# Performance work log

Measured on AMD Instinct MI355X. Metric: run time of the kernel, lower is better.

Reference implementation:

```python
import jax, jax.numpy as jnp
import numpy as np

N = 50000          # nodes
E = 800000         # edges (before self-loops)
IN = 128           # in_dim
HID = 128          # hidden_dim
HEADS = 4
G = 256            # graphs in batch
EPS = 1e-5         # batchnorm eps
NEG_SLOPE = 0.2    # GATConv leaky_relu slope


def _gat_layer(x, src, dst, W, a_src, a_dst, bias, H, C, concat):
    """PyG-style GATConv (self-loops already appended to src/dst)."""
    n = x.shape[0]
    h = (x @ W).reshape(n, H, C)                       # [N,H,C]
    s_src = (h * a_src).sum(-1)                        # [N,H]
    s_dst = (h * a_dst).sum(-1)                        # [N,H]
    e = jax.nn.leaky_relu(s_src[src] + s_dst[dst], NEG_SLOPE)   # [E',H]
    m = jax.ops.segment_max(e, dst, num_segments=n)    # segment-wise softmax
    ex = jnp.exp(e - m[dst])
    den = jax.ops.segment_sum(ex, dst, num_segments=n)
    alpha = ex / den[dst]                              # [E',H]
    out = jax.ops.segment_sum(alpha[..., None] * h[src], dst, num_segments=n)  # [N,H,C]
    out = out.reshape(n, H * C) if concat else out.mean(axis=1)
    return out + bias


def _bn(x, gamma, beta):
    # PyG BatchNorm over nodes (training-mode batch statistics)
    mu = x.mean(axis=0)
    var = x.var(axis=0)
    return gamma * (x - mu) * jax.lax.rsqrt(var + EPS) + beta


def setup_inputs() -> dict:
    key = jax.random.key(0)
    ks = jax.random.split(key, 32)
    d = {}
    d["x"] = jax.random.normal(ks[0], (N, IN), dtype=jnp.float32)
    d["edge_index"] = jax.random.randint(ks[1], (2, E), 0, N, dtype=jnp.int64)
    d["batch_idx"] = jnp.sort(jax.random.randint(ks[2], (N,), 0, G, dtype=jnp.int64))
    dims = [(IN, HEADS, HID, True), (HID * HEADS, HEADS, HID, True), (HID * HEADS, 1, HID, False)]
    for i, (din, H, C, concat) in enumerate(dims):
        d[f"W{i}"] = jax.random.normal(ks[3 + 4 * i], (din, H * C), dtype=jnp.float32) * 0.05
        d[f"att_src{i}"] = jax.random.normal(ks[4 + 4 * i], (H, C), dtype=jnp.float32) * 0.05
        d[f"att_dst{i}"] = jax.random.normal(ks[5 + 4 * i], (H, C), dtype=jnp.float32) * 0.05
        out_w = H * C if concat else C
        d[f"bias{i}"] = jnp.zeros((out_w,), dtype=jnp.float32)
        d[f"gamma{i}"] = jnp.ones((out_w,), dtype=jnp.float32)
        d[f"beta{i}"] = jnp.zeros((out_w,), dtype=jnp.float32)
    return d


def reference(x, edge_index, batch_idx,
              W0, att_src0, att_dst0, bias0, gamma0, beta0,
              W1, att_src1, att_dst1, bias1, gamma1, beta1,
              W2, att_src2, att_dst2, bias2, gamma2, beta2):
    n = x.shape[0]
    loops = jnp.arange(n, dtype=edge_index.dtype)
    src = jnp.concatenate([edge_index[0], loops])
    dst = jnp.concatenate([edge_index[1], loops])
    layers = [
        (W0, att_src0, att_dst0, bias0, gamma0, beta0, HEADS, HID, True),
        (W1, att_src1, att_dst1, bias1, gamma1, beta1, HEADS, HID, True),
        (W2, att_src2, att_dst2, bias2, gamma2, beta2, 1, HID, False),
    ]
    h = x
    for (W, a_s, a_d, b, g, bt, H, C, concat) in layers:
        h = _gat_layer(h, src, dst, W, a_s, a_d, b, H, C, concat)
        h = jax.nn.elu(_bn(h, g, bt))
        # dropout: identity in eval mode
    # global_mean_pool over batch_idx
    sums = jax.ops.segment_sum(h, batch_idx, num_segments=G)
    cnt = jax.ops.segment_sum(jnp.ones((n,), dtype=h.dtype), batch_idx, num_segments=G)
    return sums / jnp.maximum(cnt, 1.0)[:, None]
```

## Files before the change

kernel.cpp:

```cpp
#include <hip/hip_runtime.h>
#include <math.h>
#include <stdint.h>

#define N_NODES 50000
#define NPAD    50048
#define N_EDGES 800000
#define EP      (N_EDGES + N_NODES)
#define G_GRAPHS 256
#define BN_EPS   1e-5f
#define NEG_SLOPE 0.2f

typedef float f32x4 __attribute__((ext_vector_type(4)));
typedef _Float16 h16x8 __attribute__((ext_vector_type(8)));

static __device__ __forceinline__ float lrelu(float x) {
    return x > 0.f ? x : NEG_SLOPE * x;
}

static __device__ __forceinline__ void gld_lds16(const void* g, void* l) {
    __builtin_amdgcn_global_load_lds((const __attribute__((address_space(1))) void*)g,
                                     (__attribute__((address_space(3))) void*)l, 16, 0, 0);
}

static __device__ __forceinline__ float2 h2f2(unsigned u) {
    union { unsigned u; _Float16 h[2]; } c;
    c.u = u;
    return make_float2((float)c.h[0], (float)c.h[1]);
}

__global__ void k_hist(const int* __restrict__ ei, int* __restrict__ deg) {
    int stride = gridDim.x * blockDim.x;
    for (int e = blockIdx.x * blockDim.x + threadIdx.x; e < EP; e += stride) {
        int d = (e < N_EDGES) ? ei[N_EDGES + e] : (e - N_EDGES);
        atomicAdd(&deg[d], 1);
    }
}

__global__ void k_scan1(const int* __restrict__ deg, int* __restrict__ row_start,
                        int* __restrict__ totals) {
    __shared__ int buf[1024];
    int t = threadIdx.x;
    int i = blockIdx.x * 1024 + t;
    int v = (i < N_NODES) ? deg[i] : 0;
    buf[t] = v;
    __syncthreads();
    for (int off = 1; off < 1024; off <<= 1) {
        int add = (t >= off) ? buf[t - off] : 0;
        __syncthreads();
        buf[t] += add;
        __syncthreads();
    }
    if (i < N_NODES) row_start[i] = buf[t] - v;
    if (t == 1023) totals[blockIdx.x] = buf[t];
}

__global__ void k_scan2(int* __restrict__ totals, int nb) {
    if (threadIdx.x == 0 && blockIdx.x == 0) {
        int run = 0;
        for (int i = 0; i < nb; ++i) { int v = totals[i]; totals[i] = run; run += v; }
    }
}

__global__ void k_scan3(int* __restrict__ row_start, const int* __restrict__ totals) {
    int i = blockIdx.x * blockDim.x + threadIdx.x;
    if (i < N_NODES) row_start[i] += totals[i >> 10];
    if (i == 0) row_start[N_NODES] = EP;
}

__global__ void k_scatter(const int* __restrict__ ei, const int* __restrict__ row_start,
                          int* __restrict__ cursor, int* __restrict__ csr_src) {
    int stride = gridDim.x * blockDim.x;
    for (int e = blockIdx.x * blockDim.x + threadIdx.x; e < EP; e += stride) {
        int s, d;
        if (e < N_EDGES) { s = ei[e]; d = ei[N_EDGES + e]; }
        else             { s = d = e - N_EDGES; }
        int pos = row_start[d] + atomicAdd(&cursor[d], 1);
        csr_src[pos] = s;
    }
}

__global__ void k_cvtW(const float* __restrict__ W, _Float16* __restrict__ bthi,
                       int Nc, int nsh, int KS) {
    int i = blockIdx.x * 256 + threadIdx.x;
    if (i >= (KS << 5) * Nc) return;
    int k = i >> nsh;
    int n = i & (Nc - 1);
    int c = n >> 7, col = n & 127;
    int ks = k >> 5, kq = (k >> 3) & 3, j = k & 7;
    size_t idx = ((size_t)(c * KS + ks) << 12) + (kq << 10) + (col << 3) + j;
    bthi[idx] = (_Float16)W[i];
}

__global__ void k_bnprep(const float* __restrict__ bnsum, const float* __restrict__ bnsq,
                         const float* __restrict__ gamma, const float* __restrict__ beta,
                         float* __restrict__ scale, float* __restrict__ shift, int W) {
    int f = blockIdx.x * 256 + threadIdx.x;
    if (f >= W) return;
    const float invN = 1.f / (float)N_NODES;
    float mean = bnsum[f] * invN;
    float var  = bnsq[f] * invN - mean * mean;
    float sc = gamma[f] * rsqrtf(var + BN_EPS);
    scale[f] = sc;
    shift[f] = beta[f] - mean * sc;
}

__global__ void k_prepA0(const float* __restrict__ x, _Float16* __restrict__ Aswz,
                         int K, int s8, int KS) {
    int i = blockIdx.x * 256 + threadIdx.x;
    if (i >= NPAD * (K >> 3)) return;
    int r  = i >> s8;
    int c8 = i & ((K >> 3) - 1);
    int k  = c8 << 3;
    union { _Float16 h[8]; uint4 u; } pk;
    if (r < N_NODES) {
        float4 a0 = *(const float4*)&x[(size_t)r * K + k];
        float4 a1 = *(const float4*)&x[(size_t)r * K + k + 4];
        pk.h[0]=(_Float16)a0.x; pk.h[1]=(_Float16)a0.y; pk.h[2]=(_Float16)a0.z; pk.h[3]=(_Float16)a0.w;
        pk.h[4]=(_Float16)a1.x; pk.h[5]=(_Float16)a1.y; pk.h[6]=(_Float16)a1.z; pk.h[7]=(_Float16)a1.w;
    } else {
        pk.u.x = pk.u.y = pk.u.z = pk.u.w = 0u;
    }
    int rb = r >> 7, row = r & 127;
    int ks = k >> 5, kq = (k >> 3) & 3;
    size_t idx = ((size_t)(rb * KS + ks) << 12) + (kq << 10) + (row << 3);
    *(uint4*)&Aswz[idx] = pk.u;
}

__global__ void k_prepA1(const _Float16* __restrict__ act, const float* __restrict__ scale,
                         const float* __restrict__ shift, _Float16* __restrict__ Aswz,
                         int K, int s8, int KS) {
    int i = blockIdx.x * 256 + threadIdx.x;
    if (i >= NPAD * (K >> 3)) return;
    int r  = i >> s8;
    int c8 = i & ((K >> 3) - 1);
    int k  = c8 << 3;
    union { _Float16 h[8]; uint4 u; } pk;
    if (r < N_NODES) {
        uint4 v = *(const uint4*)&act[(size_t)r * K + k];
        float4 sc0 = *(const float4*)&scale[k];
        float4 sc1 = *(const float4*)&scale[k + 4];
        float4 sh0 = *(const float4*)&shift[k];
        float4 sh1 = *(const float4*)&shift[k + 4];
        float2 p0 = h2f2(v.x), p1 = h2f2(v.y), p2 = h2f2(v.z), p3 = h2f2(v.w);
        float y;
        y = fmaf(p0.x, sc0.x, sh0.x); pk.h[0] = (_Float16)(y > 0.f ? y : expm1f(y));
        y = fmaf(p0.y, sc0.y, sh0.y); pk.h[1] = (_Float16)(y > 0.f ? y : expm1f(y));
        y = fmaf(p1.x, sc0.z, sh0.z); pk.h[2] = (_Float16)(y > 0.f ? y : expm1f(y));
        y = fmaf(p1.y, sc0.w, sh0.w); pk.h[3] = (_Float16)(y > 0.f ? y : expm1f(y));
        y = fmaf(p2.x, sc1.x, sh1.x); pk.h[4] = (_Float16)(y > 0.f ? y : expm1f(y));
        y = fmaf(p2.y, sc1.y, sh1.y); pk.h[5] = (_Float16)(y > 0.f ? y : expm1f(y));
        y = fmaf(p3.x, sc1.z, sh1.z); pk.h[6] = (_Float16)(y > 0.f ? y : expm1f(y));
        y = fmaf(p3.y, sc1.w, sh1.w); pk.h[7] = (_Float16)(y > 0.f ? y : expm1f(y));
    } else {
        pk.u.x = pk.u.y = pk.u.z = pk.u.w = 0u;
    }
    int rb = r >> 7, row = r & 127;
    int ks = k >> 5, kq = (k >> 3) & 3;
    size_t idx = ((size_t)(rb * KS + ks) << 12) + (kq << 10) + (row << 3);
    *(uint4*)&Aswz[idx] = pk.u;
}

__launch_bounds__(256)
__global__ void k_gemm_f16(const _Float16* __restrict__ Aswz, const _Float16* __restrict__ bthi,
                           _Float16* __restrict__ C2,
                           float* __restrict__ sSg, float* __restrict__ sDg,
                           const float* __restrict__ asr, const float* __restrict__ adr,
                           int M, int K, int Nc) {
    __shared__ _Float16 Ah[4096], Bh[4096];
    __shared__ float rS[128], rD[128];
    const int t    = threadIdx.x;
    const int lane = t & 63, wv = t >> 6;
    const int wr = wv >> 1, wc = wv & 1;
    const int lr = lane & 15, kq = lane >> 4;
    const int r0 = blockIdx.x * 128, c0 = blockIdx.y * 128;
    const int KS = K >> 5;
    const int H = Nc >> 7;
    const int head = blockIdx.y;

    const size_t achunk0 = (size_t)blockIdx.x * KS * 4096;
    const size_t bchunk0 = (size_t)blockIdx.y * KS * 4096;

    f32x4 acc[4][4];
    #pragma unroll
    for (int m = 0; m < 4; ++m)
        #pragma unroll
        for (int n = 0; n < 4; ++n) {
            acc[m][n][0] = 0.f; acc[m][n][1] = 0.f;
            acc[m][n][2] = 0.f; acc[m][n][3] = 0.f;
        }

    for (int ks = 0; ks < KS; ++ks) {
        __syncthreads();
        const _Float16* as  = Aswz + achunk0 + ((size_t)ks << 12);
        const _Float16* bhs = bthi + bchunk0 + ((size_t)ks << 12);
        #pragma unroll
        for (int p = 0; p < 2; ++p) {
            int ge = p * 2048 + wv * 512 + lane * 8;
            int le = p * 2048 + wv * 512;
            gld_lds16(as  + ge, &Ah[le]);
            gld_lds16(bhs + ge, &Bh[le]);
        }
        __syncthreads();

        h16x8 af[4], bfh[4];
        #pragma unroll
        for (int m = 0; m < 4; ++m) {
            int row = wr * 64 + m * 16 + lr;
            af[m] = *(const h16x8*)&Ah[kq * 1024 + row * 8];
        }
        #pragma unroll
        for (int n = 0; n < 4; ++n) {
            int col = wc * 64 + n * 16 + lr;
            bfh[n] = *(const h16x8*)&Bh[kq * 1024 + col * 8];
        }
        #pragma unroll
        for (int m = 0; m < 4; ++m)
            #pragma unroll
            for (int n = 0; n < 4; ++n)
                acc[m][n] = __builtin_amdgcn_mfma_f32_16x16x32_f16(af[m], bfh[n], acc[m][n], 0, 0, 0);
    }

    float aS[4], aD[4];
    #pragma unroll
    for (int n = 0; n < 4; ++n) {
        int c = c0 + wc * 64 + n * 16 + lr;
        aS[n] = asr[c];
        aD[n] = adr[c];
    }
    __syncthreads();
    if (t < 128) { rS[t] = 0.f; rD[t] = 0.f; }
    __syncthreads();
    #pragma unroll
    for (int m = 0; m < 4; ++m) {
        #pragma unroll
        for (int j = 0; j < 4; ++j) {
            float ps = 0.f, pd = 0.f;
            #pragma unroll
            for (int n = 0; n < 4; ++n) {
                float v = acc[m][n][j];
                ps += v * aS[n];
                pd += v * aD[n];
            }
            #pragma unroll
            for (int off = 1; off < 16; off <<= 1) {
                ps += __shfl_xor(ps, off, 64);
                pd += __shfl_xor(pd, off, 64);
            }
            if (lr == 0) {
                int row = wr * 64 + m * 16 + kq * 4 + j;
                atomicAdd(&rS[row], ps);
                atomicAdd(&rD[row], pd);
            }
        }
    }
    __syncthreads();
    if (t < 128) {
        int r = r0 + t;
        if (r < M) {
            sSg[(size_t)r * H + head] = rS[t];
            sDg[(size_t)r * H + head] = rD[t];
        }
    }

    #pragma unroll
    for (int m = 0; m < 4; ++m) {
        int rowb = r0 + wr * 64 + m * 16 + kq * 4;
        #pragma unroll
        for (int n = 0; n < 4; ++n) {
            int col = c0 + wc * 64 + n * 16 + lr;
            #pragma unroll
            for (int j = 0; j < 4; ++j) {
                int r = rowb + j;
                if (r < M) C2[(size_t)r * Nc + col] = (_Float16)acc[m][n][j];
            }
        }
    }
}

template<int H, int CPT, int CAP>
__launch_bounds__(256)
__global__ void k_attnagg(const _Float16* __restrict__ hb2, const float* __restrict__ s_src,
                          const float* __restrict__ s_dst, const int* __restrict__ row_start,
                          const int* __restrict__ csr, const float* __restrict__ bias,
                          _Float16* __restrict__ out) {
    const int W = H * 128;
    __shared__ float alds[4][CAP * H];
    const int wv = threadIdx.x >> 6;
    const int lane = threadIdx.x & 63;
    const int n = blockIdx.x * 4 + wv;
    if (n >= N_NODES) return;
    const int lo = row_start[n], hi = row_start[n + 1];
    const int deg = hi - lo;

    const int h1 = lane & (H - 1);
    const int eo = lane / H;
    const int EPI = 64 / H;
    float sd1 = s_dst[n * H + h1];
    const int c0 = lane * CPT;
    const int myh = c0 >> 7;

    float acc[CPT];
    #pragma unroll
    for (int j = 0; j < CPT; ++j) acc[j] = 0.f;

    if (deg <= CAP) {
        float* al = &alds[wv][0];
        float mx = -INFINITY;
        for (int q = eo; q < deg; q += EPI) {
            float e = lrelu(s_src[csr[lo + q] * H + h1] + sd1);
            al[q * H + h1] = e;
            mx = fmaxf(mx, e);
        }
        #pragma unroll
        for (int off = H; off < 64; off <<= 1) mx = fmaxf(mx, __shfl_xor(mx, off, 64));
        float sum = 0.f;
        for (int q = eo; q < deg; q += EPI) {
            float ex = expf(al[q * H + h1] - mx);
            al[q * H + h1] = ex;
            sum += ex;
        }
        #pragma unroll
        for (int off = H; off < 64; off <<= 1) sum += __shfl_xor(sum, off, 64);
        float invv = __shfl(1.f / sum, myh, 64);
        asm volatile("s_waitcnt lgkmcnt(0)" ::: "memory");
        __builtin_amdgcn_sched_barrier(0);

        int q = 0;
        for (; q + 8 <= deg; q += 8) {
            int s[8];
            #pragma unroll
            for (int j = 0; j < 8; ++j) s[j] = csr[lo + q + j];
            float a[8];
            #pragma unroll
            for (int j = 0; j < 8; ++j) a[j] = al[(q + j) * H + myh];
            if constexpr (CPT == 8) {
                uint4 v[8];
                #pragma unroll
                for (int j = 0; j < 8; ++j) v[j] = *(const uint4*)&hb2[(size_t)s[j] * W + c0];
                #pragma unroll
                for (int j = 0; j < 8; ++j) {
                    float2 x0 = h2f2(v[j].x), x1 = h2f2(v[j].y), x2 = h2f2(v[j].z), x3 = h2f2(v[j].w);
                    acc[0] += a[j]*x0.x; acc[1] += a[j]*x0.y; acc[2] += a[j]*x1.x; acc[3] += a[j]*x1.y;
                    acc[4] += a[j]*x2.x; acc[5] += a[j]*x2.y; acc[6] += a[j]*x3.x; acc[7] += a[j]*x3.y;
                }
            } else {
                unsigned v[8];
                #pragma unroll
                for (int j = 0; j < 8; ++j) v[j] = *(const unsigned*)&hb2[(size_t)s[j] * W + c0];
                #pragma unroll
                for (int j = 0; j < 8; ++j) {
                    float2 x = h2f2(v[j]);
                    acc[0] += a[j]*x.x; acc[1] += a[j]*x.y;
                }
            }
        }
        for (; q < deg; ++q) {
            int s0 = csr[lo + q];
            float a0 = al[q * H + myh];
            if constexpr (CPT == 8) {
                uint4 v0 = *(const uint4*)&hb2[(size_t)s0 * W + c0];
                float2 x0 = h2f2(v0.x), x1 = h2f2(v0.y), x2 = h2f2(v0.z), x3 = h2f2(v0.w);
                acc[0] += a0*x0.x; acc[1] += a0*x0.y; acc[2] += a0*x1.x; acc[3] += a0*x1.y;
                acc[4] += a0*x2.x; acc[5] += a0*x2.y; acc[6] += a0*x3.x; acc[7] += a0*x3.y;
            } else {
                float2 x = h2f2(*(const unsigned*)&hb2[(size_t)s0 * W + c0]);
                acc[0] += a0*x.x; acc[1] += a0*x.y;
            }
        }

        union { _Float16 h[CPT]; uint4 u4; unsigned u1; } pk;
        #pragma unroll
        for (int j = 0; j < CPT; ++j) pk.h[j] = (_Float16)(fmaf(acc[j], invv, bias[c0 + j]));
        if constexpr (CPT == 8)
            *(uint4*)&out[(size_t)n * W + c0] = pk.u4;
        else
            *(unsigned*)&out[(size_t)n * W + c0] = pk.u1;
        return;
    }

    float mx = -INFINITY;
    for (int p = lo + eo; p < hi; p += EPI) {
        float e = lrelu(s_src[csr[p] * H + h1] + sd1);
        mx = fmaxf(mx, e);
    }
    #pragma unroll
    for (int off = H; off < 64; off <<= 1) mx = fmaxf(mx, __shfl_xor(mx, off, 64));
    float sum = 0.f;
    for (int p = lo + eo; p < hi; p += EPI) {
        float e = lrelu(s_src[csr[p] * H + h1] + sd1);
        sum += expf(e - mx);
    }
    #pragma unroll
    for (int off = H; off < 64; off <<= 1) sum += __shfl_xor(sum, off, 64);
    float inv = 1.f / sum;

    float mxv  = __shfl(mx,  myh, 64);
    float invv = __shfl(inv, myh, 64);
    float sdv  = __shfl(sd1, myh, 64);

    for (int p = lo; p < hi; ++p) {
        int s0 = csr[p];
        float a0 = expf(lrelu(s_src[s0 * H + myh] + sdv) - mxv);
        if constexpr (CPT == 8) {
            uint4 v0 = *(const uint4*)&hb2[(size_t)s0 * W + c0];
            float2 x0 = h2f2(v0.x), x1 = h2f2(v0.y), x2 = h2f2(v0.z), x3 = h2f2(v0.w);
            acc[0] += a0*x0.x; acc[1] += a0*x0.y; acc[2] += a0*x1.x; acc[3] += a0*x1.y;
            acc[4] += a0*x2.x; acc[5] += a0*x2.y; acc[6] += a0*x3.x; acc[7] += a0*x3.y;
        } else {
            float2 x = h2f2(*(const unsigned*)&hb2[(size_t)s0 * W + c0]);
            acc[0] += a0*x.x; acc[1] += a0*x.y;
        }
    }
    union { _Float16 h[CPT]; uint4 u4; unsigned u1; } pk;
    #pragma unroll
    for (int j = 0; j < CPT; ++j) pk.h[j] = (_Float16)(fmaf(acc[j], invv, bias[c0 + j]));
    if constexpr (CPT == 8)
        *(uint4*)&out[(size_t)n * W + c0] = pk.u4;
    else
        *(unsigned*)&out[(size_t)n * W + c0] = pk.u1;
}

__global__ void k_bnstat2(const _Float16* __restrict__ x, float* __restrict__ bnsum,
                          float* __restrict__ bnsq, int W) {
    const int RPB = 64;
    int t  = threadIdx.x;
    int r0 = blockIdx.x * RPB;
    int r1 = min(r0 + RPB, N_NODES);
    float s0 = 0.f, q0 = 0.f, s1 = 0.f, q1 = 0.f;
    for (int r = r0; r < r1; ++r) {
        float2 v = h2f2(*(const unsigned*)&x[(size_t)r * W + 2 * t]);
        s0 += v.x; q0 += v.x * v.x;
        s1 += v.y; q1 += v.y * v.y;
    }
    atomicAdd(&bnsum[2*t],   s0);
    atomicAdd(&bnsq[2*t],    q0);
    atomicAdd(&bnsum[2*t+1], s1);
    atomicAdd(&bnsq[2*t+1],  q1);
}

__global__ void k_pool(const _Float16* __restrict__ x, const int* __restrict__ batch,
                       const float* __restrict__ scale, const float* __restrict__ shift,
                       float* __restrict__ out) {
    int g = blockIdx.x;
    int f = threadIdx.x;
    int a = 0, b = N_NODES;
    while (a < b) { int m = (a + b) >> 1; if (batch[m] < g) a = m + 1; else b = m; }
    int lo = a;
    b = N_NODES;
    while (a < b) { int m = (a + b) >> 1; if (batch[m] < g + 1) a = m + 1; else b = m; }
    int hi = a;
    float sc = scale[f], sh = shift[f];
    float s = 0.f;
    for (int r = lo; r < hi; ++r) {
        float v = (float)x[(size_t)r * 128 + f];
        float y = fmaf(v, sc, sh);
        s += (y > 0.f) ? y : expm1f(y);
    }
    int cnt = hi - lo;
    out[g * 128 + f] = s / (float)(cnt > 0 ? cnt : 1);
}

extern "C" void kernel_launch(void* const* d_in, const int* in_sizes, int n_in,
                              void* d_out, int out_size, void* d_ws, size_t ws_size,
                              hipStream_t stream) {
    const float* x     = (const float*)d_in[0];
    const int*   ei    = (const int*)d_in[1];
    const int*   batch = (const int*)d_in[2];
    const float* Wm[3]  = {(const float*)d_in[3],  (const float*)d_in[9],  (const float*)d_in[15]};
    const float* asr[3] = {(const float*)d_in[4],  (const float*)d_in[10], (const float*)d_in[16]};
    const float* adr[3] = {(const float*)d_in[5],  (const float*)d_in[11], (const float*)d_in[17]};
    const float* bia[3] = {(const float*)d_in[6],  (const float*)d_in[12], (const float*)d_in[18]};
    const float* gam[3] = {(const float*)d_in[7],  (const float*)d_in[13], (const float*)d_in[19]};
    const float* bet[3] = {(const float*)d_in[8],  (const float*)d_in[14], (const float*)d_in[20]};

    char* w = (char*)d_ws;
    auto alloc = [&](size_t bytes) -> void* {
        void* p = (void*)w;
        w += (bytes + 255) & ~(size_t)255;
        return p;
    };
    _Float16* act2   = (_Float16*)alloc((size_t)N_NODES * 512 * 2);
    _Float16* act128 = (_Float16*)alloc((size_t)N_NODES * 128 * 2);
    _Float16* hb2    = (_Float16*)alloc((size_t)N_NODES * 512 * 2);
    _Float16* Aswz   = (_Float16*)alloc((size_t)NPAD * 512 * 2);
    int* csr_src   = (int*)alloc((size_t)EP * 4);
    int* row_start = (int*)alloc((size_t)(N_NODES + 1) * 4);
    int* deg       = (int*)alloc((size_t)N_NODES * 4);
    int* cursor    = (int*)alloc((size_t)N_NODES * 4);
    float* s_src = (float*)alloc((size_t)N_NODES * 4 * 4);
    float* s_dst = (float*)alloc((size_t)N_NODES * 4 * 4);
    float* bn    = (float*)alloc(1024 * 4);
    float* scl   = (float*)alloc(512 * 4);
    float* shf   = (float*)alloc(512 * 4);
    int* totals  = (int*)alloc(64 * 4);
    _Float16* bthi = (_Float16*)alloc((size_t)512 * 512 * 2);

    hipMemsetAsync(deg, 0, (size_t)N_NODES * 4, stream);
    hipMemsetAsync(cursor, 0, (size_t)N_NODES * 4, stream);
    k_hist<<<512, 256, 0, stream>>>(ei, deg);
    k_scan1<<<(N_NODES + 1023) / 1024, 1024, 0, stream>>>(deg, row_start, totals);
    k_scan2<<<1, 64, 0, stream>>>(totals, (N_NODES + 1023) / 1024);
    k_scan3<<<(N_NODES + 255) / 256, 256, 0, stream>>>(row_start, totals);
    k_scatter<<<512, 256, 0, stream>>>(ei, row_start, cursor, csr_src);

    auto layer = [&](int K, int li, int H, bool first, _Float16* outAct) {
        int Wd = H * 128;
        int nsh = (Wd == 512) ? 9 : 7;
        int KS = K >> 5;
        int s8 = (K == 512) ? 6 : 4;
        int tot = K * Wd;
        k_cvtW<<<(tot + 255) / 256, 256, 0, stream>>>(Wm[li], bthi, Wd, nsh, KS);
        int ptot = NPAD * (K >> 3);
        if (first)
            k_prepA0<<<(ptot + 255) / 256, 256, 0, stream>>>(x, Aswz, K, s8, KS);
        else
            k_prepA1<<<(ptot + 255) / 256, 256, 0, stream>>>(act2, scl, shf, Aswz, K, s8, KS);
        dim3 gg(NPAD / 128, Wd / 128);
        k_gemm_f16<<<gg, 256, 0, stream>>>(Aswz, bthi, hb2, s_src, s_dst,
                                           asr[li], adr[li], N_NODES, K, Wd);
        int nb = (N_NODES + 3) / 4;
        if (H == 4)
            k_attnagg<4, 8, 256><<<nb, 256, 0, stream>>>(hb2, s_src, s_dst, row_start, csr_src,
                                                         bia[li], outAct);
        else
            k_attnagg<1, 2, 256><<<nb, 256, 0, stream>>>(hb2, s_src, s_dst, row_start, csr_src,
                                                         bia[li], outAct);
        hipMemsetAsync(bn, 0, 1024 * 4, stream);
        k_bnstat2<<<(N_NODES + 63) / 64, Wd / 2, 0, stream>>>(outAct, bn, bn + 512, Wd);
        k_bnprep<<<(Wd + 255) / 256, 256, 0, stream>>>(bn, bn + 512, gam[li], bet[li], scl, shf, Wd);
    };

    layer(128, 0, 4, true,  act2);
    layer(512, 1, 4, false, act2);
    layer(512, 2, 1, false, act128);

    k_pool<<<G_GRAPHS, 128, 0, stream>>>(act128, batch, scl, shf, (float*)d_out);
}
```

Before: 853.4 us.

## Fold BN-prep into consumers and make attention aggregation a persistent grid-stride kernel

Removes the separate k_bnprep kernel. Its scale/shift computation is now redone inline in k_prepA1 and k_pool from the raw BN sums, which saves three kernel launches at the cost of extra redundant per-thread math. The attention-aggregation kernel now launches a fixed grid of 2048 blocks that grid-stride over node groups, instead of one block per four nodes. This cuts block-scheduling overhead but may affect load balance across nodes with very different degrees.

Result: slower. 1.165 ms (+36.5%).

```diff
diff --git a/kernel.cpp b/kernel.cpp
--- a/kernel.cpp
+++ b/kernel.cpp
@@ -89,19 +89,6 @@
     int ks = k >> 5, kq = (k >> 3) & 3, j = k & 7;
     size_t idx = ((size_t)(c * KS + ks) << 12) + (kq << 10) + (col << 3) + j;
     bthi[idx] = (_Float16)W[i];
-}
-
-__global__ void k_bnprep(const float* __restrict__ bnsum, const float* __restrict__ bnsq,
-                         const float* __restrict__ gamma, const float* __restrict__ beta,
-                         float* __restrict__ scale, float* __restrict__ shift, int W) {
-    int f = blockIdx.x * 256 + threadIdx.x;
-    if (f >= W) return;
-    const float invN = 1.f / (float)N_NODES;
-    float mean = bnsum[f] * invN;
-    float var  = bnsq[f] * invN - mean * mean;
-    float sc = gamma[f] * rsqrtf(var + BN_EPS);
-    scale[f] = sc;
-    shift[f] = beta[f] - mean * sc;
 }
 
 __global__ void k_prepA0(const float* __restrict__ x, _Float16* __restrict__ Aswz,
@@ -126,31 +113,30 @@
     *(uint4*)&Aswz[idx] = pk.u;
 }
 
-__global__ void k_prepA1(const _Float16* __restrict__ act, const float* __restrict__ scale,
-                         const float* __restrict__ shift, _Float16* __restrict__ Aswz,
+__global__ void k_prepA1(const _Float16* __restrict__ act, const float* __restrict__ bnsum,
+                         const float* __restrict__ bnsq, const float* __restrict__ gamma,
+                         const float* __restrict__ beta, _Float16* __restrict__ Aswz,
                          int K, int s8, int KS) {
     int i = blockIdx.x * 256 + threadIdx.x;
     if (i >= NPAD * (K >> 3)) return;
     int r  = i >> s8;
     int c8 = i & ((K >> 3) - 1);
     int k  = c8 << 3;
+    const float invN = 1.f / (float)N_NODES;
     union { _Float16 h[8]; uint4 u; } pk;
     if (r < N_NODES) {
         uint4 v = *(const uint4*)&act[(size_t)r * K + k];
-        float4 sc0 = *(const float4*)&scale[k];
-        float4 sc1 = *(const float4*)&scale[k + 4];
-        float4 sh0 = *(const float4*)&shift[k];
-        float4 sh1 = *(const float4*)&shift[k + 4];
-        float2 p0 = h2f2(v.x), p1 = h2f2(v.y), p2 = h2f2(v.z), p3 = h2f2(v.w);
-        float y;
-        y = fmaf(p0.x, sc0.x, sh0.x); pk.h[0] = (_Float16)(y > 0.f ? y : expm1f(y));
-        y = fmaf(p0.y, sc0.y, sh0.y); pk.h[1] = (_Float16)(y > 0.f ? y : expm1f(y));
-        y = fmaf(p1.x, sc0.z, sh0.z); pk.h[2] = (_Float16)(y > 0.f ? y : expm1f(y));
-        y = fmaf(p1.y, sc0.w, sh0.w); pk.h[3] = (_Float16)(y > 0.f ? y : expm1f(y));
-        y = fmaf(p2.x, sc1.x, sh1.x); pk.h[4] = (_Float16)(y > 0.f ? y : expm1f(y));
-        y = fmaf(p2.y, sc1.y, sh1.y); pk.h[5] = (_Float16)(y > 0.f ? y : expm1f(y));
-        y = fmaf(p3.x, sc1.z, sh1.z); pk.h[6] = (_Float16)(y > 0.f ? y : expm1f(y));
-        y = fmaf(p3.y, sc1.w, sh1.w); pk.h[7] = (_Float16)(y > 0.f ? y : expm1f(y));
+        float2 p[4] = {h2f2(v.x), h2f2(v.y), h2f2(v.z), h2f2(v.w)};
+        float vin[8] = {p[0].x, p[0].y, p[1].x, p[1].y, p[2].x, p[2].y, p[3].x, p[3].y};
+        #pragma unroll
+        for (int j = 0; j < 8; ++j) {
+            float mean = bnsum[k + j] * invN;
+            float var  = bnsq[k + j] * invN - mean * mean;
+            float sc = gamma[k + j] * rsqrtf(var + BN_EPS);
+            float sh = beta[k + j] - mean * sc;
+            float y = fmaf(vin[j], sc, sh);
+            pk.h[j] = (_Float16)(y > 0.f ? y : expm1f(y));
+        }
     } else {
         pk.u.x = pk.u.y = pk.u.z = pk.u.w = 0u;
     }
@@ -287,84 +273,120 @@
     __shared__ float alds[4][CAP * H];
     const int wv = threadIdx.x >> 6;
     const int lane = threadIdx.x & 63;
-    const int n = blockIdx.x * 4 + wv;
-    if (n >= N_NODES) return;
-    const int lo = row_start[n], hi = row_start[n + 1];
-    const int deg = hi - lo;
-
     const int h1 = lane & (H - 1);
     const int eo = lane / H;
     const int EPI = 64 / H;
-    float sd1 = s_dst[n * H + h1];
     const int c0 = lane * CPT;
     const int myh = c0 >> 7;
-
-    float acc[CPT];
-    #pragma unroll
-    for (int j = 0; j < CPT; ++j) acc[j] = 0.f;
-
-    if (deg <= CAP) {
-        float* al = &alds[wv][0];
-        float mx = -INFINITY;
-        for (int q = eo; q < deg; q += EPI) {
-            float e = lrelu(s_src[csr[lo + q] * H + h1] + sd1);
-            al[q * H + h1] = e;
-            mx = fmaxf(mx, e);
-        }
-        #pragma unroll
-        for (int off = H; off < 64; off <<= 1) mx = fmaxf(mx, __shfl_xor(mx, off, 64));
-        float sum = 0.f;
-        for (int q = eo; q < deg; q += EPI) {
-            float ex = expf(al[q * H + h1] - mx);
-            al[q * H + h1] = ex;
-            sum += ex;
-        }
-        #pragma unroll
-        for (int off = H; off < 64; off <<= 1) sum += __shfl_xor(sum, off, 64);
-        float invv = __shfl(1.f / sum, myh, 64);
-        asm volatile("s_waitcnt lgkmcnt(0)" ::: "memory");
-        __builtin_amdgcn_sched_barrier(0);
-
-        int q = 0;
-        for (; q + 8 <= deg; q += 8) {
-            int s[8];
-            #pragma unroll
-            for (int j = 0; j < 8; ++j) s[j] = csr[lo + q + j];
-            float a[8];
-            #pragma unroll
-            for (int j = 0; j < 8; ++j) a[j] = al[(q + j) * H + myh];
-            if constexpr (CPT == 8) {
-                uint4 v[8];
+    const int ngroups = (N_NODES + 3) >> 2;
+    float* al = &alds[wv][0];
+
+    for (int grp = blockIdx.x; grp < ngroups; grp += gridDim.x) {
+        const int n = grp * 4 + wv;
+        if (n >= N_NODES) continue;
+        const int lo = row_start[n], hi = row_start[n + 1];
+        const int deg = hi - lo;
+        float sd1 = s_dst[n * H + h1];
+
+        float acc[CPT];
+        #pragma unroll
+        for (int j = 0; j < CPT; ++j) acc[j] = 0.f;
+        float invv;
+
+        if (deg <= CAP) {
+            float mx = -INFINITY;
+            for (int q = eo; q < deg; q += EPI) {
+                float e = lrelu(s_src[csr[lo + q] * H + h1] + sd1);
+                al[q * H + h1] = e;
+                mx = fmaxf(mx, e);
+            }
+            #pragma unroll
+            for (int off = H; off < 64; off <<= 1) mx = fmaxf(mx, __shfl_xor(mx, off, 64));
+            float sum = 0.f;
+            for (int q = eo; q < deg; q += EPI) {
+                float ex = expf(al[q * H + h1] - mx);
+                al[q * H + h1] = ex;
+                sum += ex;
+            }
+            #pragma unroll
+            for (int off = H; off < 64; off <<= 1) sum += __shfl_xor(sum, off, 64);
+            invv = __shfl(1.f / sum, myh, 64);
+            asm volatile("s_waitcnt lgkmcnt(0)" ::: "memory");
+            __builtin_amdgcn_sched_barrier(0);
+
+            int q = 0;
+            for (; q + 8 <= deg; q += 8) {
+                int s[8];
                 #pragma unroll
-                for (int j = 0; j < 8; ++j) v[j] = *(const uint4*)&hb2[(size_t)s[j] * W + c0];
+                for (int j = 0; j < 8; ++j) s[j] = csr[lo + q + j];
+                float a[8];
                 #pragma unroll
-                for (int j = 0; j < 8; ++j) {
-                    float2 x0 = h2f2(v[j].x), x1 = h2f2(v[j].y), x2 = h2f2(v[j].z), x3 = h2f2(v[j].w);
-                    acc[0] += a[j]*x0.x; acc[1] += a[j]*x0.y; acc[2] += a[j]*x1.x; acc[3] += a[j]*x1.y;
-                    acc[4] += a[j]*x2.x; acc[5] += a[j]*x2.y; acc[6] += a[j]*x3.x; acc[7] += a[j]*x3.y;
+                for (int j = 0; j < 8; ++j) a[j] = al[(q + j) * H + myh];
+                if constexpr (CPT == 8) {
+                    uint4 v[8];
+                    #pragma unroll
+                    for (int j = 0; j < 8; ++j) v[j] = *(const uint4*)&hb2[(size_t)s[j] * W + c0];
+                    #pragma unroll
+                    for (int j = 0; j < 8; ++j) {
+                        float2 x0 = h2f2(v[j].x), x1 = h2f2(v[j].y), x2 = h2f2(v[j].z), x3 = h2f2(v[j].w);
+                        acc[0] += a[j]*x0.x; acc[1] += a[j]*x0.y; acc[2] += a[j]*x1.x; acc[3] += a[j]*x1.y;
+                        acc[4] += a[j]*x2.x; acc[5] += a[j]*x2.y; acc[6] += a[j]*x3.x; acc[7] += a[j]*x3.y;
+                    }
+                } else {
+                    unsigned v[8];
+                    #pragma unroll
+                    for (int j = 0; j < 8; ++j) v[j] = *(const unsigned*)&hb2[(size_t)s[j] * W + c0];
+                    #pragma unroll
+                    for (int j = 0; j < 8; ++j) {
+                        float2 x = h2f2(v[j]);
+                        acc[0] += a[j]*x.x; acc[1] += a[j]*x.y;
+                    }
                 }
-            } else {
-                unsigned v[8];
-                #pragma unroll
-                for (int j = 0; j < 8; ++j) v[j] = *(const unsigned*)&hb2[(size_t)s[j] * W + c0];
-                #pragma unroll
-                for (int j = 0; j < 8; ++j) {
-                    float2 x = h2f2(v[j]);
-                    acc[0] += a[j]*x.x; acc[1] += a[j]*x.y;
+            }
+            for (; q < deg; ++q) {
+                int s0 = csr[lo + q];
+                float a0 = al[q * H + myh];
+                if constexpr (CPT == 8) {
+                    uint4 v0 = *(const uint4*)&hb2[(size_t)s0 * W + c0];
+                    float2 x0 = h2f2(v0.x), x1 = h2f2(v0.y), x2 = h2f2(v0.z), x3 = h2f2(v0.w);
+                    acc[0] += a0*x0.x; acc[1] += a0*x0.y; acc[2] += a0*x1.x; acc[3] += a0*x1.y;
+                    acc[4] += a0*x2.x; acc[5] += a0*x2.y; acc[6] += a0*x3.x; acc[7] += a0*x3.y;
+                } else {
+                    float2 x = h2f2(*(const unsigned*)&hb2[(size_t)s0 * W + c0]);
+                    acc[0] += a0*x.x; acc[1] += a0*x.y;
                 }
             }
-        }
-        for (; q < deg; ++q) {
-            int s0 = csr[lo + q];
-            float a0 = al[q * H + myh];
-            if constexpr (CPT == 8) {
-                uint4 v0 = *(const uint4*)&hb2[(size_t)s0 * W + c0];
-                float2 x0 = h2f2(v0.x), x1 = h2f2(v0.y), x2 = h2f2(v0.z), x3 = h2f2(v0.w);
-                acc[0] += a0*x0.x; acc[1] += a0*x0.y; acc[2] += a0*x1.x; acc[3] += a0*x1.y;
-                acc[4] += a0*x2.x; acc[5] += a0*x2.y; acc[6] += a0*x3.x; acc[7] += a0*x3.y;
-            } else {
-                float2 x = h2f2(*(const unsigned*)&hb2[(size_t)s0 * W + c0]);
-                acc[0] += a0*x.x; acc[1] += a0*x.y;
+        } else {
+            float mx = -INFINITY;
+            for (int p = lo + eo; p < hi; p += EPI) {
+                float e = lrelu(s_src[csr[p] * H + h1] + sd1);
+                mx = fmaxf(mx, e);
+            }
+            #pragma unroll
+            for (int off = H; off < 64; off <<= 1) mx = fmaxf(mx, __shfl_xor(mx, off, 64));
+            float sum = 0.f;
+            for (int p = lo + eo; p < hi; p += EPI) {
+                float e = lrelu(s_src[csr[p] * H + h1] + sd1);
+                sum += expf(e - mx);
+            }
+            #pragma unroll
+            for (int off = H; off < 64; off <<= 1) sum += __shfl_xor(sum, off, 64);
+            float inv = 1.f / sum;
+            float mxv = __shfl(mx, myh, 64);
+            invv = __shfl(inv, myh, 64);
+            float sdv = __shfl(sd1, myh, 64);
+            for (int p = lo; p < hi; ++p) {
+                int s0 = csr[p];
+                float a0 = expf(lrelu(s_src[s0 * H + myh] + sdv) - mxv);
+                if constexpr (CPT == 8) {
+                    uint4 v0 = *(const uint4*)&hb2[(size_t)s0 * W + c0];
+                    float2 x0 = h2f2(v0.x), x1 = h2f2(v0.y), x2 = h2f2(v0.z), x3 = h2f2(v0.w);
+                    acc[0] += a0*x0.x; acc[1] += a0*x0.y; acc[2] += a0*x1.x; acc[3] += a0*x1.y;
+                    acc[4] += a0*x2.x; acc[5] += a0*x2.y; acc[6] += a0*x3.x; acc[7] += a0*x3.y;
+                } else {
+                    float2 x = h2f2(*(const unsigned*)&hb2[(size_t)s0 * W + c0]);
+                    acc[0] += a0*x.x; acc[1] += a0*x.y;
+                }
             }
         }
 
@@ -375,49 +397,7 @@
             *(uint4*)&out[(size_t)n * W + c0] = pk.u4;
         else
             *(unsigned*)&out[(size_t)n * W + c0] = pk.u1;
-        return;
-    }
-
-    float mx = -INFINITY;
-    for (int p = lo + eo; p < hi; p += EPI) {
-        float e = lrelu(s_src[csr[p] * H + h1] + sd1);
-        mx = fmaxf(mx, e);
-    }
-    #pragma unroll
-    for (int off = H; off < 64; off <<= 1) mx = fmaxf(mx, __shfl_xor(mx, off, 64));
-    float sum = 0.f;
-    for (int p = lo + eo; p < hi; p += EPI) {
-        float e = lrelu(s_src[csr[p] * H + h1] + sd1);
-        sum += expf(e - mx);
-    }
-    #pragma unroll
-    for (int off = H; off < 64; off <<= 1) sum += __shfl_xor(sum, off, 64);
-    float inv = 1.f / sum;
-
-    float mxv  = __shfl(mx,  myh, 64);
-    float invv = __shfl(inv, myh, 64);
-    float sdv  = __shfl(sd1, myh, 64);
-
-    for (int p = lo; p < hi; ++p) {
-        int s0 = csr[p];
-        float a0 = expf(lrelu(s_src[s0 * H + myh] + sdv) - mxv);
-        if constexpr (CPT == 8) {
-            uint4 v0 = *(const uint4*)&hb2[(size_t)s0 * W + c0];
-            float2 x0 = h2f2(v0.x), x1 = h2f2(v0.y), x2 = h2f2(v0.z), x3 = h2f2(v0.w);
-            acc[0] += a0*x0.x; acc[1] += a0*x0.y; acc[2] += a0*x1.x; acc[3] += a0*x1.y;
-            acc[4] += a0*x2.x; acc[5] += a0*x2.y; acc[6] += a0*x3.x; acc[7] += a0*x3.y;
-        } else {
-            float2 x = h2f2(*(const unsigned*)&hb2[(size_t)s0 * W + c0]);
-            acc[0] += a0*x.x; acc[1] += a0*x.y;
-        }
-    }
-    union { _Float16 h[CPT]; uint4 u4; unsigned u1; } pk;
-    #pragma unroll
-    for (int j = 0; j < CPT; ++j) pk.h[j] = (_Float16)(fmaf(acc[j], invv, bias[c0 + j]));
-    if constexpr (CPT == 8)
-        *(uint4*)&out[(size_t)n * W + c0] = pk.u4;
-    else
-        *(unsigned*)&out[(size_t)n * W + c0] = pk.u1;
+    }
 }
 
 __global__ void k_bnstat2(const _Float16* __restrict__ x, float* __restrict__ bnsum,
@@ -439,17 +419,22 @@
 }
 
 __global__ void k_pool(const _Float16* __restrict__ x, const int* __restrict__ batch,
-                       const float* __restrict__ scale, const float* __restrict__ shift,
+                       const float* __restrict__ bnsum, const float* __restrict__ bnsq,
+                       const float* __restrict__ gamma, const float* __restrict__ beta,
                        float* __restrict__ out) {
     int g = blockIdx.x;
     int f = threadIdx.x;
+    const float invN = 1.f / (float)N_NODES;
+    float mean = bnsum[f] * invN;
+    float var  = bnsq[f] * invN - mean * mean;
+    float sc = gamma[f] * rsqrtf(var + BN_EPS);
+    float sh = beta[f] - mean * sc;
     int a = 0, b = N_NODES;
     while (a < b) { int m = (a + b) >> 1; if (batch[m] < g) a = m + 1; else b = m; }
     int lo = a;
     b = N_NODES;
     while (a < b) { int m = (a + b) >> 1; if (batch[m] < g + 1) a = m + 1; else b = m; }
     int hi = a;
-    float sc = scale[f], sh = shift[f];
     float s = 0.f;
     for (int r = lo; r < hi; ++r) {
         float v = (float)x[(size_t)r * 128 + f];
@@ -490,8 +475,6 @@
     float* s_src = (float*)alloc((size_t)N_NODES * 4 * 4);
     float* s_dst = (float*)alloc((size_t)N_NODES * 4 * 4);
     float* bn    = (float*)alloc(1024 * 4);
-    float* scl   = (float*)alloc(512 * 4);
-    float* shf   = (float*)alloc(512 * 4);
     int* totals  = (int*)alloc(64 * 4);
     _Float16* bthi = (_Float16*)alloc((size_t)512 * 512 * 2);
 
@@ -514,25 +497,25 @@
         if (first)
             k_prepA0<<<(ptot + 255) / 256, 256, 0, stream>>>(x, Aswz, K, s8, KS);
         else
-            k_prepA1<<<(ptot + 255) / 256, 256, 0, stream>>>(act2, scl, shf, Aswz, K, s8, KS);
+            k_prepA1<<<(ptot + 255) / 256, 256, 0, stream>>>(act2, bn, bn + 512,
+                                                             gam[li - 1], bet[li - 1],
+                                                             Aswz, K, s8, KS);
         dim3 gg(NPAD / 128, Wd / 128);
         k_gemm_f16<<<gg, 256, 0, stream>>>(Aswz, bthi, hb2, s_src, s_dst,
                                            asr[li], adr[li], N_NODES, K, Wd);
-        int nb = (N_NODES + 3) / 4;
         if (H == 4)
-            k_attnagg<4, 8, 256><<<nb, 256, 0, stream>>>(hb2, s_src, s_dst, row_start, csr_src,
-                                                         bia[li], outAct);
+            k_attnagg<4, 8, 256><<<2048, 256, 0, stream>>>(hb2, s_src, s_dst, row_start, csr_src,
+                                                           bia[li], outAct);
         else
-            k_attnagg<1, 2, 256><<<nb, 256, 0, stream>>>(hb2, s_src, s_dst, row_start, csr_src,
-                                                         bia[li], outAct);
+            k_attnagg<1, 2, 256><<<2048, 256, 0, stream>>>(hb2, s_src, s_dst, row_start, csr_src,
+                                                           bia[li], outAct);
         hipMemsetAsync(bn, 0, 1024 * 4, stream);
         k_bnstat2<<<(N_NODES + 63) / 64, Wd / 2, 0, stream>>>(outAct, bn, bn + 512, Wd);
-        k_bnprep<<<(Wd + 255) / 256, 256, 0, stream>>>(bn, bn + 512, gam[li], bet[li], scl, shf, Wd);
     };
 
     layer(128, 0, 4, true,  act2);
     layer(512, 1, 4, false, act2);
     layer(512, 2, 1, false, act128);
 
-    k_pool<<<G_GRAPHS, 128, 0, stream>>>(act128, batch, scl, shf, (float*)d_out);
-}
+    k_pool<<<G_GRAPHS, 128, 0, stream>>>(act128, batch, bn, bn + 512, gam[2], bet[2], (float*)d_out);
+}
```
